# Performance work log

Measured on AMD Instinct MI355X. Metric: run time of the kernel, lower is better.

## Reference

```python
import jax, jax.numpy as jnp
import numpy as np

B, T, S, F, H, V = 4, 160, 80, 640, 1024, 1024

def setup_inputs() -> dict:
    key = jax.random.key(0)
    ks = jax.random.split(key, 4)
    return {
        "source_encodings": jax.random.normal(ks[0], (B, T, F), dtype=jnp.float32),
        "target_encodings": jax.random.normal(ks[1], (B, S, F), dtype=jnp.float32),
        "W1": jax.random.normal(ks[2], (F, H), dtype=jnp.float32) * (1.0 / np.sqrt(F)),
        "b1": jnp.zeros((H,), dtype=jnp.float32),
        "W2": jax.random.normal(ks[3], (H, V), dtype=jnp.float32) * (1.0 / np.sqrt(H)),
        "b2": jnp.zeros((V,), dtype=jnp.float32),
    }

def reference(source_encodings, target_encodings, W1, b1, W2, b2):
    # broadcast add: [B,T,1,F] + [B,1,S,F] -> [B,T,S,F]
    combined = source_encodings[:, :, None, :] + target_encodings[:, None, :, :]
    # FFN: Linear -> ReLU -> Linear (dropout=0 / eval)
    h = jax.nn.relu(jnp.einsum("btsf,fh->btsh", combined, W1) + b1)
    logits = jnp.einsum("btsh,hv->btsv", h, W2) + b2
    # eval mode applies log_softmax over vocab
    return jax.nn.log_softmax(logits, axis=-1)
```

## Files before the change

kernel.cpp:

```cpp
#include <hip/hip_runtime.h>
#include <type_traits>
#include <utility>

#define B_ 4
#define T_ 160
#define S_ 80
#define F_ 640
#define H_ 1024
#define V_ 1024

typedef float f32x4 __attribute__((ext_vector_type(4)));
typedef short s16x8 __attribute__((ext_vector_type(8)));
typedef __bf16 bf16x8_t __attribute__((ext_vector_type(8)));

template <typename T, typename = void>
struct MfmaTakes : std::false_type {};
template <typename T>
struct MfmaTakes<T, std::void_t<decltype(__builtin_amdgcn_mfma_f32_16x16x32_bf16(
    std::declval<T>(), std::declval<T>(), std::declval<f32x4>(), 0, 0, 0))>>
    : std::true_type {};

template <typename S8>
__device__ __forceinline__ f32x4 mfma_bf16_16x16x32(S8 a, S8 b, f32x4 c) {
  if constexpr (MfmaTakes<S8>::value) {
    return __builtin_amdgcn_mfma_f32_16x16x32_bf16(a, b, c, 0, 0, 0);
  } else {
    return __builtin_amdgcn_mfma_f32_16x16x32_bf16(
        __builtin_bit_cast(bf16x8_t, a), __builtin_bit_cast(bf16x8_t, b), c, 0, 0, 0);
  }
}

__device__ __forceinline__ unsigned short f2bf(float x) {
  unsigned int u = __float_as_uint(x);
  u += 0x7FFFu + ((u >> 16) & 1u);
  return (unsigned short)(u >> 16);
}

__global__ __launch_bounds__(256) void prep_weights(const float* __restrict__ W1,
                                                    const float* __restrict__ W2,
                                                    s16x8* __restrict__ W1p,
                                                    s16x8* __restrict__ W2p) {
  const int NW1 = (F_ / 8) * H_;
  const int NW2 = (H_ / 8) * V_;
  int c = blockIdx.x * 256 + threadIdx.x;
  if (c < NW1) {
    int kg = c >> 10, v = c & 1023;
    s16x8 o;
#pragma unroll
    for (int i = 0; i < 8; ++i) o[i] = (short)f2bf(W1[(kg * 8 + i) * H_ + v]);
    W1p[c] = o;
  } else if (c < NW1 + NW2) {
    int c2 = c - NW1;
    int kg = c2 >> 10, v = c2 & 1023;
    s16x8 o;
#pragma unroll
    for (int i = 0; i < 8; ++i) o[i] = (short)f2bf(W2[(kg * 8 + i) * V_ + v]);
    W2p[c2] = o;
  }
}

__global__ __launch_bounds__(512, 2) void pq_gemm(const float* __restrict__ src,
                                                  const float* __restrict__ tgt,
                                                  const s16x8* __restrict__ W1p,
                                                  const float* __restrict__ b1,
                                                  float* __restrict__ P,
                                                  float* __restrict__ Q) {
  __shared__ s16x8 a_lds[64 * 80];
  const int tid = threadIdx.x;
  const int wr = blockIdx.x;
  const int r0 = wr * 64;
  const bool isP = (wr < 10);

  for (int c = tid; c < 64 * 80; c += 512) {
    int m = c / 80, kg8 = c - m * 80;
    int R = r0 + m;
    const float* rowp = isP ? (src + R * F_) : (tgt + (R - 640) * F_);
    const f32x4* p4 = (const f32x4*)(rowp + kg8 * 8);
    f32x4 x0 = p4[0], x1 = p4[1];
    s16x8 o;
#pragma unroll
    for (int i = 0; i < 4; ++i) o[i] = (short)f2bf(x0[i]);
#pragma unroll
    for (int i = 0; i < 4; ++i) o[4 + i] = (short)f2bf(x1[i]);
    a_lds[m * 80 + (kg8 ^ (m & 7))] = o;
  }
  __syncthreads();

  const int l = tid & 63, wv = tid >> 6;
  const int g = l >> 4, cl = l & 15;
  const f32x4 zero = {0.f, 0.f, 0.f, 0.f};
  f32x4 acc[4][8];
#pragma unroll
  for (int rt = 0; rt < 4; ++rt)
#pragma unroll
    for (int ct = 0; ct < 8; ++ct) acc[rt][ct] = zero;

  const s16x8* bbase = W1p + g * 1024 + wv * 128 + cl;
  s16x8 bA[8], bB[8], af[4];
#pragma unroll
  for (int ct = 0; ct < 8; ++ct) bA[ct] = bbase[ct * 16];

  for (int ks = 0; ks < 20; ks += 2) {
#pragma unroll
    for (int ct = 0; ct < 8; ++ct) bB[ct] = bbase[(ks + 1) * 4096 + ct * 16];
#pragma unroll
    for (int rt = 0; rt < 4; ++rt) {
      int m = rt * 16 + cl;
      af[rt] = a_lds[m * 80 + ((ks * 4 + g) ^ (m & 7))];
    }
#pragma unroll
    for (int ct = 0; ct < 8; ++ct)
#pragma unroll
      for (int rt = 0; rt < 4; ++rt)
        acc[rt][ct] = mfma_bf16_16x16x32(af[rt], bA[ct], acc[rt][ct]);
    int ksn = (ks + 2 < 20) ? (ks + 2) : 0;
#pragma unroll
    for (int ct = 0; ct < 8; ++ct) bA[ct] = bbase[ksn * 4096 + ct * 16];
#pragma unroll
    for (int rt = 0; rt < 4; ++rt) {
      int m = rt * 16 + cl;
      af[rt] = a_lds[m * 80 + (((ks + 1) * 4 + g) ^ (m & 7))];
    }
#pragma unroll
    for (int ct = 0; ct < 8; ++ct)
#pragma unroll
      for (int rt = 0; rt < 4; ++rt)
        acc[rt][ct] = mfma_bf16_16x16x32(af[rt], bB[ct], acc[rt][ct]);
  }

  float b1v[8];
#pragma unroll
  for (int ct = 0; ct < 8; ++ct) b1v[ct] = isP ? b1[wv * 128 + ct * 16 + cl] : 0.f;
  float* outbase = isP ? P : Q;
  const int orow0 = isP ? r0 : (r0 - 640);
#pragma unroll
  for (int rt = 0; rt < 4; ++rt) {
#pragma unroll
    for (int j = 0; j < 4; ++j) {
      int row = rt * 16 + g * 4 + j;
      float* op = outbase + (size_t)(orow0 + row) * H_ + wv * 128 + cl;
#pragma unroll
      for (int ct = 0; ct < 8; ++ct) op[ct * 16] = acc[rt][ct][j] + b1v[ct];
    }
  }
}

__global__ __launch_bounds__(512, 2) void joint_main(const float* __restrict__ Pm,
                                                     const float* __restrict__ Qm,
                                                     const s16x8* __restrict__ W2p,
                                                     const float* __restrict__ b2,
                                                     float* __restrict__ out) {
  __shared__ s16x8 h_lds[32 * 129];
  const int tid = threadIdx.x;
  int bx = blockIdx.x;
  int bid = (bx & 7) * 200 + (bx >> 3);
  const int b = bid / 400;
  int rem = bid - b * 400;
  const int t0 = (rem / 10) * 4;
  const int s0 = (rem - (rem / 10) * 10) * 8;

  for (int c = tid; c < 32 * 128; c += 512) {
    int m = c >> 7, kg8 = c & 127;
    int dt = m >> 3, ds = m & 7;
    const f32x4* p4 = (const f32x4*)(Pm + (size_t)(b * T_ + t0 + dt) * H_ + kg8 * 8);
    const f32x4* q4 = (const f32x4*)(Qm + (size_t)(b * S_ + s0 + ds) * H_ + kg8 * 8);
    f32x4 x0 = p4[0] + q4[0];
    f32x4 x1 = p4[1] + q4[1];
    s16x8 o;
#pragma unroll
    for (int i = 0; i < 4; ++i) o[i] = (short)f2bf(fmaxf(x0[i], 0.f));
#pragma unroll
    for (int i = 0; i < 4; ++i) o[4 + i] = (short)f2bf(fmaxf(x1[i], 0.f));
    h_lds[m * 129 + kg8] = o;
  }
  __syncthreads();

  const int l = tid & 63, wv = tid >> 6;
  const int g = l >> 4, cl = l & 15;
  f32x4 acc[2][8];
#pragma unroll
  for (int rt = 0; rt < 2; ++rt)
#pragma unroll
    for (int ct = 0; ct < 8; ++ct) acc[rt][ct] = {0.f, 0.f, 0.f, 0.f};

  const s16x8* bb = W2p + g * 1024 + wv * 128 + cl;
  const s16x8* a0p = h_lds + cl * 129 + g;
  const s16x8* a1p = h_lds + (16 + cl) * 129 + g;

  s16x8 b0[4], b1[4], af0, af1;
#pragma unroll
  for (int i = 0; i < 4; ++i) b0[i] = bb[i * 16];
  af0 = a0p[0];
  af1 = a1p[0];

#pragma unroll
  for (int ks = 0; ks < 32; ++ks) {
#pragma unroll
    for (int i = 0; i < 4; ++i) b1[i] = bb[ks * 4096 + 64 + i * 16];
    __builtin_amdgcn_s_setprio(1);
#pragma unroll
    for (int i = 0; i < 4; ++i) {
      acc[0][i] = mfma_bf16_16x16x32(af0, b0[i], acc[0][i]);
      acc[1][i] = mfma_bf16_16x16x32(af1, b0[i], acc[1][i]);
    }
    __builtin_amdgcn_s_setprio(0);
    const int ksn = (ks + 1 < 32) ? ks + 1 : 0;
#pragma unroll
    for (int i = 0; i < 4; ++i) b0[i] = bb[ksn * 4096 + i * 16];
    s16x8 afn0 = a0p[ksn * 4];
    s16x8 afn1 = a1p[ksn * 4];
    __builtin_amdgcn_s_setprio(1);
#pragma unroll
    for (int i = 0; i < 4; ++i) {
      acc[0][4 + i] = mfma_bf16_16x16x32(af0, b1[i], acc[0][4 + i]);
      acc[1][4 + i] = mfma_bf16_16x16x32(af1, b1[i], acc[1][4 + i]);
    }
    __builtin_amdgcn_s_setprio(0);
    af0 = afn0;
    af1 = afn1;
  }

  __syncthreads();
  float* redm = reinterpret_cast<float*>(h_lds);
  float* reds = redm + 256;
  float* gmbuf = reds + 256;
  float* lsebuf = gmbuf + 32;

#pragma unroll
  for (int ct = 0; ct < 8; ++ct) {
    float bv = b2[wv * 128 + ct * 16 + cl];
#pragma unroll
    for (int rt = 0; rt < 2; ++rt)
#pragma unroll
      for (int j = 0; j < 4; ++j) acc[rt][ct][j] += bv;
  }

#pragma unroll
  for (int rt = 0; rt < 2; ++rt)
#pragma unroll
    for (int j = 0; j < 4; ++j) {
      float mx = acc[rt][0][j];
#pragma unroll
      for (int ct = 1; ct < 8; ++ct) mx = fmaxf(mx, acc[rt][ct][j]);
#pragma unroll
      for (int msk = 1; msk < 16; msk <<= 1) mx = fmaxf(mx, __shfl_xor(mx, msk, 64));
      if (cl == 0) redm[wv * 32 + rt * 16 + g * 4 + j] = mx;
    }
  __syncthreads();

  if (tid < 32) {
    float mx = redm[tid];
#pragma unroll
    for (int w = 1; w < 8; ++w) mx = fmaxf(mx, redm[w * 32 + tid]);
    gmbuf[tid] = mx;
  }
  __syncthreads();

#pragma unroll
  for (int rt = 0; rt < 2; ++rt)
#pragma unroll
    for (int j = 0; j < 4; ++j) {
      int row = rt * 16 + g * 4 + j;
      float gm = gmbuf[row];
      float ps = 0.f;
#pragma unroll
      for (int ct = 0; ct < 8; ++ct) ps += __expf(acc[rt][ct][j] - gm);
#pragma unroll
      for (int msk = 1; msk < 16; msk <<= 1) ps += __shfl_xor(ps, msk, 64);
      if (cl == 0) reds[wv * 32 + row] = ps;
    }
  __syncthreads();

  if (tid < 32) {
    float s = reds[tid];
#pragma unroll
    for (int w = 1; w < 8; ++w) s += reds[w * 32 + tid];
    lsebuf[tid] = gmbuf[tid] + __logf(s);
  }
  __syncthreads();

#pragma unroll
  for (int rt = 0; rt < 2; ++rt)
#pragma unroll
    for (int j = 0; j < 4; ++j) {
      int row = rt * 16 + g * 4 + j;
      float lse = lsebuf[row];
      int n = (b * T_ + t0 + (row >> 3)) * S_ + s0 + (row & 7);
      float* op = out + (size_t)n * V_ + wv * 128 + cl;
#pragma unroll
      for (int ct = 0; ct < 8; ++ct) op[ct * 16] = acc[rt][ct][j] - lse;
    }
}

extern "C" void kernel_launch(void* const* d_in, const int* in_sizes, int n_in,
                              void* d_out, int out_size, void* d_ws, size_t ws_size,
                              hipStream_t stream) {
  const float* src = (const float*)d_in[0];
  const float* tgt = (const float*)d_in[1];
  const float* W1  = (const float*)d_in[2];
  const float* b1  = (const float*)d_in[3];
  const float* W2  = (const float*)d_in[4];
  const float* b2  = (const float*)d_in[5];
  float* out = (float*)d_out;

  char* ws = (char*)d_ws;
  s16x8* W1p = (s16x8*)(ws);
  s16x8* W2p = (s16x8*)(ws + 1310720);
  float* P   = (float*)(ws + 3407872);
  float* Q   = (float*)(ws + 6029312);

  prep_weights<<<832, 256, 0, stream>>>(W1, W2, W1p, W2p);
  pq_gemm<<<15, 512, 0, stream>>>(src, tgt, W1p, b1, P, Q);
  joint_main<<<1600, 512, 0, stream>>>(P, Q, W2p, b2, out);
}
```

Before: 201.2 us.

## Double the joint kernel's row tile to 64 rows per block to reuse W2

Each joint_main block now handles 8 t by 8 s (64 output rows) instead of 4 by 8, so every W2 fragment loaded from global memory feeds four MFMA row tiles instead of two. This halves total W2 traffic, and the grid drops from 1600 to 800 blocks. The B-fragment prefetch is restructured into full 8-wide current/next buffers, and the setprio interleaving is removed. The cost is roughly double the accumulator and fragment registers and LDS, which may drop occupancy below the declared 2 blocks per CU or cause spills, plus fewer blocks to balance across CUs.

```diff
diff --git a/kernel.cpp b/kernel.cpp
--- a/kernel.cpp
+++ b/kernel.cpp
@@ -150,16 +150,16 @@
                                                      const s16x8* __restrict__ W2p,
                                                      const float* __restrict__ b2,
                                                      float* __restrict__ out) {
-  __shared__ s16x8 h_lds[32 * 129];
+  __shared__ s16x8 h_lds[64 * 129];
   const int tid = threadIdx.x;
   int bx = blockIdx.x;
-  int bid = (bx & 7) * 200 + (bx >> 3);
-  const int b = bid / 400;
-  int rem = bid - b * 400;
-  const int t0 = (rem / 10) * 4;
+  int bid = (bx & 7) * 100 + (bx >> 3);
+  const int b = bid / 200;
+  int rem = bid - b * 200;
+  const int t0 = (rem / 10) * 8;
   const int s0 = (rem - (rem / 10) * 10) * 8;
 
-  for (int c = tid; c < 32 * 128; c += 512) {
+  for (int c = tid; c < 64 * 128; c += 512) {
     int m = c >> 7, kg8 = c & 127;
     int dt = m >> 3, ds = m & 7;
     const f32x4* p4 = (const f32x4*)(Pm + (size_t)(b * T_ + t0 + dt) * H_ + kg8 * 8);
@@ -177,66 +177,59 @@
 
   const int l = tid & 63, wv = tid >> 6;
   const int g = l >> 4, cl = l & 15;
-  f32x4 acc[2][8];
-#pragma unroll
-  for (int rt = 0; rt < 2; ++rt)
+  f32x4 acc[4][8];
+#pragma unroll
+  for (int rt = 0; rt < 4; ++rt)
 #pragma unroll
     for (int ct = 0; ct < 8; ++ct) acc[rt][ct] = {0.f, 0.f, 0.f, 0.f};
 
   const s16x8* bb = W2p + g * 1024 + wv * 128 + cl;
-  const s16x8* a0p = h_lds + cl * 129 + g;
-  const s16x8* a1p = h_lds + (16 + cl) * 129 + g;
-
-  s16x8 b0[4], b1[4], af0, af1;
-#pragma unroll
-  for (int i = 0; i < 4; ++i) b0[i] = bb[i * 16];
-  af0 = a0p[0];
-  af1 = a1p[0];
-
-#pragma unroll
+  const s16x8* a0p = h_lds + (0 * 16 + cl) * 129 + g;
+  const s16x8* a1p = h_lds + (1 * 16 + cl) * 129 + g;
+  const s16x8* a2p = h_lds + (2 * 16 + cl) * 129 + g;
+  const s16x8* a3p = h_lds + (3 * 16 + cl) * 129 + g;
+
+  s16x8 bcur[8], bnxt[8], af[4], afn[4];
+#pragma unroll
+  for (int i = 0; i < 8; ++i) bcur[i] = bb[i * 16];
+  af[0] = a0p[0]; af[1] = a1p[0]; af[2] = a2p[0]; af[3] = a3p[0];
+
+#pragma unroll 4
   for (int ks = 0; ks < 32; ++ks) {
-#pragma unroll
-    for (int i = 0; i < 4; ++i) b1[i] = bb[ks * 4096 + 64 + i * 16];
-    __builtin_amdgcn_s_setprio(1);
-#pragma unroll
-    for (int i = 0; i < 4; ++i) {
-      acc[0][i] = mfma_bf16_16x16x32(af0, b0[i], acc[0][i]);
-      acc[1][i] = mfma_bf16_16x16x32(af1, b0[i], acc[1][i]);
-    }
-    __builtin_amdgcn_s_setprio(0);
     const int ksn = (ks + 1 < 32) ? ks + 1 : 0;
-#pragma unroll
-    for (int i = 0; i < 4; ++i) b0[i] = bb[ksn * 4096 + i * 16];
-    s16x8 afn0 = a0p[ksn * 4];
-    s16x8 afn1 = a1p[ksn * 4];
-    __builtin_amdgcn_s_setprio(1);
-#pragma unroll
-    for (int i = 0; i < 4; ++i) {
-      acc[0][4 + i] = mfma_bf16_16x16x32(af0, b1[i], acc[0][4 + i]);
-      acc[1][4 + i] = mfma_bf16_16x16x32(af1, b1[i], acc[1][4 + i]);
-    }
-    __builtin_amdgcn_s_setprio(0);
-    af0 = afn0;
-    af1 = afn1;
+    const s16x8* nb = bb + ksn * 4096;
+#pragma unroll
+    for (int i = 0; i < 8; ++i) bnxt[i] = nb[i * 16];
+    afn[0] = a0p[ksn * 4]; afn[1] = a1p[ksn * 4];
+    afn[2] = a2p[ksn * 4]; afn[3] = a3p[ksn * 4];
+#pragma unroll
+    for (int ct = 0; ct < 8; ++ct)
+#pragma unroll
+      for (int rt = 0; rt < 4; ++rt)
+        acc[rt][ct] = mfma_bf16_16x16x32(af[rt], bcur[ct], acc[rt][ct]);
+#pragma unroll
+    for (int i = 0; i < 8; ++i) bcur[i] = bnxt[i];
+#pragma unroll
+    for (int rt = 0; rt < 4; ++rt) af[rt] = afn[rt];
   }
 
   __syncthreads();
   float* redm = reinterpret_cast<float*>(h_lds);
-  float* reds = redm + 256;
-  float* gmbuf = reds + 256;
-  float* lsebuf = gmbuf + 32;
+  float* reds = redm + 512;
+  float* gmbuf = reds + 512;
+  float* lsebuf = gmbuf + 64;
 
 #pragma unroll
   for (int ct = 0; ct < 8; ++ct) {
     float bv = b2[wv * 128 + ct * 16 + cl];
 #pragma unroll
-    for (int rt = 0; rt < 2; ++rt)
+    for (int rt = 0; rt < 4; ++rt)
 #pragma unroll
       for (int j = 0; j < 4; ++j) acc[rt][ct][j] += bv;
   }
 
 #pragma unroll
-  for (int rt = 0; rt < 2; ++rt)
+  for (int rt = 0; rt < 4; ++rt)
 #pragma unroll
     for (int j = 0; j < 4; ++j) {
       float mx = acc[rt][0][j];
@@ -244,20 +237,20 @@
       for (int ct = 1; ct < 8; ++ct) mx = fmaxf(mx, acc[rt][ct][j]);
 #pragma unroll
       for (int msk = 1; msk < 16; msk <<= 1) mx = fmaxf(mx, __shfl_xor(mx, msk, 64));
-      if (cl == 0) redm[wv * 32 + rt * 16 + g * 4 + j] = mx;
-    }
-  __syncthreads();
-
-  if (tid < 32) {
+      if (cl == 0) redm[wv * 64 + rt * 16 + g * 4 + j] = mx;
+    }
+  __syncthreads();
+
+  if (tid < 64) {
     float mx = redm[tid];
 #pragma unroll
-    for (int w = 1; w < 8; ++w) mx = fmaxf(mx, redm[w * 32 + tid]);
+    for (int w = 1; w < 8; ++w) mx = fmaxf(mx, redm[w * 64 + tid]);
     gmbuf[tid] = mx;
   }
   __syncthreads();
 
 #pragma unroll
-  for (int rt = 0; rt < 2; ++rt)
+  for (int rt = 0; rt < 4; ++rt)
 #pragma unroll
     for (int j = 0; j < 4; ++j) {
       int row = rt * 16 + g * 4 + j;
@@ -267,20 +260,20 @@
       for (int ct = 0; ct < 8; ++ct) ps += __expf(acc[rt][ct][j] - gm);
 #pragma unroll
       for (int msk = 1; msk < 16; msk <<= 1) ps += __shfl_xor(ps, msk, 64);
-      if (cl == 0) reds[wv * 32 + row] = ps;
-    }
-  __syncthreads();
-
-  if (tid < 32) {
+      if (cl == 0) reds[wv * 64 + row] = ps;
+    }
+  __syncthreads();
+
+  if (tid < 64) {
     float s = reds[tid];
 #pragma unroll
-    for (int w = 1; w < 8; ++w) s += reds[w * 32 + tid];
+    for (int w = 1; w < 8; ++w) s += reds[w * 64 + tid];
     lsebuf[tid] = gmbuf[tid] + __logf(s);
   }
   __syncthreads();
 
 #pragma unroll
-  for (int rt = 0; rt < 2; ++rt)
+  for (int rt = 0; rt < 4; ++rt)
 #pragma unroll
     for (int j = 0; j < 4; ++j) {
       int row = rt * 16 + g * 4 + j;
@@ -311,5 +304,5 @@
 
   prep_weights<<<832, 256, 0, stream>>>(W1, W2, W1p, W2p);
   pq_gemm<<<15, 512, 0, stream>>>(src, tgt, W1p, b1, P, Q);
-  joint_main<<<1600, 512, 0, stream>>>(P, Q, W2p, b2, out);
-}
+  joint_main<<<800, 512, 0, stream>>>(P, Q, W2p, b2, out);
+}
```

After: 280.8 us. +39.6%, slower.

## Split joint_main vocab across 16 waves and drop manual software pipelining

Applied to the files above, without the earlier changes.

joint_main now launches 1024 threads per block, so each of 16 waves covers 64 vocab columns instead of 8 waves covering 128. The accumulator footprint halves, the launch bounds move to (1024, 8), and the reduction buffers grow to hold 16 per-wave partials. The hand-written double-buffered B/A prefetch and s_setprio hints are replaced by a plain loop with unroll 2, leaving load scheduling to the compiler. The aim is more resident waves to hide W2 load latency, at the cost of losing explicit prefetch overlap and adding a longer cross-wave reduction.

```diff
diff --git a/kernel.cpp b/kernel.cpp
--- a/kernel.cpp
+++ b/kernel.cpp
@@ -145,11 +145,11 @@
   }
 }
 
-__global__ __launch_bounds__(512, 2) void joint_main(const float* __restrict__ Pm,
-                                                     const float* __restrict__ Qm,
-                                                     const s16x8* __restrict__ W2p,
-                                                     const float* __restrict__ b2,
-                                                     float* __restrict__ out) {
+__global__ __launch_bounds__(1024, 8) void joint_main(const float* __restrict__ Pm,
+                                                      const float* __restrict__ Qm,
+                                                      const s16x8* __restrict__ W2p,
+                                                      const float* __restrict__ b2,
+                                                      float* __restrict__ out) {
   __shared__ s16x8 h_lds[32 * 129];
   const int tid = threadIdx.x;
   int bx = blockIdx.x;
@@ -159,7 +159,7 @@
   const int t0 = (rem / 10) * 4;
   const int s0 = (rem - (rem / 10) * 10) * 8;
 
-  for (int c = tid; c < 32 * 128; c += 512) {
+  for (int c = tid; c < 32 * 128; c += 1024) {
     int m = c >> 7, kg8 = c & 127;
     int dt = m >> 3, ds = m & 7;
     const f32x4* p4 = (const f32x4*)(Pm + (size_t)(b * T_ + t0 + dt) * H_ + kg8 * 8);
@@ -177,58 +177,44 @@
 
   const int l = tid & 63, wv = tid >> 6;
   const int g = l >> 4, cl = l & 15;
-  f32x4 acc[2][8];
-#pragma unroll
-  for (int rt = 0; rt < 2; ++rt)
-#pragma unroll
-    for (int ct = 0; ct < 8; ++ct) acc[rt][ct] = {0.f, 0.f, 0.f, 0.f};
-
-  const s16x8* bb = W2p + g * 1024 + wv * 128 + cl;
+  f32x4 acc[2][4];
+#pragma unroll
+  for (int rt = 0; rt < 2; ++rt)
+#pragma unroll
+    for (int ct = 0; ct < 4; ++ct) acc[rt][ct] = {0.f, 0.f, 0.f, 0.f};
+
+  const s16x8* bb = W2p + g * 1024 + wv * 64 + cl;
   const s16x8* a0p = h_lds + cl * 129 + g;
   const s16x8* a1p = h_lds + (16 + cl) * 129 + g;
 
-  s16x8 b0[4], b1[4], af0, af1;
-#pragma unroll
-  for (int i = 0; i < 4; ++i) b0[i] = bb[i * 16];
-  af0 = a0p[0];
-  af1 = a1p[0];
-
-#pragma unroll
+#pragma unroll 2
   for (int ks = 0; ks < 32; ++ks) {
-#pragma unroll
-    for (int i = 0; i < 4; ++i) b1[i] = bb[ks * 4096 + 64 + i * 16];
-    __builtin_amdgcn_s_setprio(1);
-#pragma unroll
-    for (int i = 0; i < 4; ++i) {
-      acc[0][i] = mfma_bf16_16x16x32(af0, b0[i], acc[0][i]);
-      acc[1][i] = mfma_bf16_16x16x32(af1, b0[i], acc[1][i]);
-    }
-    __builtin_amdgcn_s_setprio(0);
-    const int ksn = (ks + 1 < 32) ? ks + 1 : 0;
-#pragma unroll
-    for (int i = 0; i < 4; ++i) b0[i] = bb[ksn * 4096 + i * 16];
-    s16x8 afn0 = a0p[ksn * 4];
-    s16x8 afn1 = a1p[ksn * 4];
-    __builtin_amdgcn_s_setprio(1);
-#pragma unroll
-    for (int i = 0; i < 4; ++i) {
-      acc[0][4 + i] = mfma_bf16_16x16x32(af0, b1[i], acc[0][4 + i]);
-      acc[1][4 + i] = mfma_bf16_16x16x32(af1, b1[i], acc[1][4 + i]);
-    }
-    __builtin_amdgcn_s_setprio(0);
-    af0 = afn0;
-    af1 = afn1;
+    const s16x8* base = bb + ks * 4096;
+    s16x8 bf0 = base[0];
+    s16x8 bf1 = base[16];
+    s16x8 bf2 = base[32];
+    s16x8 bf3 = base[48];
+    s16x8 a0 = a0p[ks * 4];
+    s16x8 a1 = a1p[ks * 4];
+    acc[0][0] = mfma_bf16_16x16x32(a0, bf0, acc[0][0]);
+    acc[1][0] = mfma_bf16_16x16x32(a1, bf0, acc[1][0]);
+    acc[0][1] = mfma_bf16_16x16x32(a0, bf1, acc[0][1]);
+    acc[1][1] = mfma_bf16_16x16x32(a1, bf1, acc[1][1]);
+    acc[0][2] = mfma_bf16_16x16x32(a0, bf2, acc[0][2]);
+    acc[1][2] = mfma_bf16_16x16x32(a1, bf2, acc[1][2]);
+    acc[0][3] = mfma_bf16_16x16x32(a0, bf3, acc[0][3]);
+    acc[1][3] = mfma_bf16_16x16x32(a1, bf3, acc[1][3]);
   }
 
   __syncthreads();
   float* redm = reinterpret_cast<float*>(h_lds);
-  float* reds = redm + 256;
-  float* gmbuf = reds + 256;
+  float* reds = redm + 512;
+  float* gmbuf = reds + 512;
   float* lsebuf = gmbuf + 32;
 
 #pragma unroll
-  for (int ct = 0; ct < 8; ++ct) {
-    float bv = b2[wv * 128 + ct * 16 + cl];
+  for (int ct = 0; ct < 4; ++ct) {
+    float bv = b2[wv * 64 + ct * 16 + cl];
 #pragma unroll
     for (int rt = 0; rt < 2; ++rt)
 #pragma unroll
@@ -239,9 +225,8 @@
   for (int rt = 0; rt < 2; ++rt)
 #pragma unroll
     for (int j = 0; j < 4; ++j) {
-      float mx = acc[rt][0][j];
-#pragma unroll
-      for (int ct = 1; ct < 8; ++ct) mx = fmaxf(mx, acc[rt][ct][j]);
+      float mx = fmaxf(fmaxf(acc[rt][0][j], acc[rt][1][j]),
+                       fmaxf(acc[rt][2][j], acc[rt][3][j]));
 #pragma unroll
       for (int msk = 1; msk < 16; msk <<= 1) mx = fmaxf(mx, __shfl_xor(mx, msk, 64));
       if (cl == 0) redm[wv * 32 + rt * 16 + g * 4 + j] = mx;
@@ -251,7 +236,7 @@
   if (tid < 32) {
     float mx = redm[tid];
 #pragma unroll
-    for (int w = 1; w < 8; ++w) mx = fmaxf(mx, redm[w * 32 + tid]);
+    for (int w = 1; w < 16; ++w) mx = fmaxf(mx, redm[w * 32 + tid]);
     gmbuf[tid] = mx;
   }
   __syncthreads();
@@ -262,9 +247,8 @@
     for (int j = 0; j < 4; ++j) {
       int row = rt * 16 + g * 4 + j;
       float gm = gmbuf[row];
-      float ps = 0.f;
-#pragma unroll
-      for (int ct = 0; ct < 8; ++ct) ps += __expf(acc[rt][ct][j] - gm);
+      float ps = __expf(acc[rt][0][j] - gm) + __expf(acc[rt][1][j] - gm) +
+                 __expf(acc[rt][2][j] - gm) + __expf(acc[rt][3][j] - gm);
 #pragma unroll
       for (int msk = 1; msk < 16; msk <<= 1) ps += __shfl_xor(ps, msk, 64);
       if (cl == 0) reds[wv * 32 + row] = ps;
@@ -274,7 +258,7 @@
   if (tid < 32) {
     float s = reds[tid];
 #pragma unroll
-    for (int w = 1; w < 8; ++w) s += reds[w * 32 + tid];
+    for (int w = 1; w < 16; ++w) s += reds[w * 32 + tid];
     lsebuf[tid] = gmbuf[tid] + __logf(s);
   }
   __syncthreads();
@@ -286,9 +270,9 @@
       int row = rt * 16 + g * 4 + j;
       float lse = lsebuf[row];
       int n = (b * T_ + t0 + (row >> 3)) * S_ + s0 + (row & 7);
-      float* op = out + (size_t)n * V_ + wv * 128 + cl;
-#pragma unroll
-      for (int ct = 0; ct < 8; ++ct) op[ct * 16] = acc[rt][ct][j] - lse;
+      float* op = out + (size_t)n * V_ + wv * 64 + cl;
+#pragma unroll
+      for (int ct = 0; ct < 4; ++ct) op[ct * 16] = acc[rt][ct][j] - lse;
     }
 }
 
@@ -311,5 +295,5 @@
 
   prep_weights<<<832, 256, 0, stream>>>(W1, W2, W1p, W2p);
   pq_gemm<<<15, 512, 0, stream>>>(src, tgt, W1p, b1, P, Q);
-  joint_main<<<1600, 512, 0, stream>>>(P, Q, W2p, b2, out);
-}
+  joint_main<<<1600, 1024, 0, stream>>>(P, Q, W2p, b2, out);
+}
```

Measured after the change: 254.3 us. 26.4% more time.

## Split P/Q projection GEMM into 120 smaller tiles for more parallelism

Applied to the files above, without the earlier changes.

The P/Q projection GEMM previously ran on only 15 workgroups with 64-row by 1024-column tiles each. It is now split into 32-row by 256-column tiles across 120 workgroups so more compute units take part. The LDS layout changes from an XOR swizzle to a padded row stride of 81. The trade-off is that each workgroup re-converts its A rows once per column tile, and the explicit double-buffered B prefetch is removed.

```diff
diff --git a/kernel.cpp b/kernel.cpp
--- a/kernel.cpp
+++ b/kernel.cpp
@@ -65,84 +65,65 @@
                                                   const float* __restrict__ b1,
                                                   float* __restrict__ P,
                                                   float* __restrict__ Q) {
-  __shared__ s16x8 a_lds[64 * 80];
+  __shared__ s16x8 a_lds[32 * 81];
   const int tid = threadIdx.x;
-  const int wr = blockIdx.x;
-  const int r0 = wr * 64;
-  const bool isP = (wr < 10);
-
-  for (int c = tid; c < 64 * 80; c += 512) {
+  const int wg = blockIdx.x;
+  const int rowtile = wg >> 2, coltile = wg & 3;
+  const int r0 = rowtile * 32;
+  const bool isP = (r0 < 640);
+  const float* rowbase = isP ? (src + (size_t)r0 * F_) : (tgt + (size_t)(r0 - 640) * F_);
+
+  for (int c = tid; c < 32 * 80; c += 512) {
     int m = c / 80, kg8 = c - m * 80;
-    int R = r0 + m;
-    const float* rowp = isP ? (src + R * F_) : (tgt + (R - 640) * F_);
-    const f32x4* p4 = (const f32x4*)(rowp + kg8 * 8);
+    const f32x4* p4 = (const f32x4*)(rowbase + (size_t)m * F_ + kg8 * 8);
     f32x4 x0 = p4[0], x1 = p4[1];
     s16x8 o;
 #pragma unroll
     for (int i = 0; i < 4; ++i) o[i] = (short)f2bf(x0[i]);
 #pragma unroll
     for (int i = 0; i < 4; ++i) o[4 + i] = (short)f2bf(x1[i]);
-    a_lds[m * 80 + (kg8 ^ (m & 7))] = o;
+    a_lds[m * 81 + kg8] = o;
   }
   __syncthreads();
 
   const int l = tid & 63, wv = tid >> 6;
   const int g = l >> 4, cl = l & 15;
-  const f32x4 zero = {0.f, 0.f, 0.f, 0.f};
-  f32x4 acc[4][8];
-#pragma unroll
-  for (int rt = 0; rt < 4; ++rt)
-#pragma unroll
-    for (int ct = 0; ct < 8; ++ct) acc[rt][ct] = zero;
-
-  const s16x8* bbase = W1p + g * 1024 + wv * 128 + cl;
-  s16x8 bA[8], bB[8], af[4];
-#pragma unroll
-  for (int ct = 0; ct < 8; ++ct) bA[ct] = bbase[ct * 16];
-
-  for (int ks = 0; ks < 20; ks += 2) {
-#pragma unroll
-    for (int ct = 0; ct < 8; ++ct) bB[ct] = bbase[(ks + 1) * 4096 + ct * 16];
-#pragma unroll
-    for (int rt = 0; rt < 4; ++rt) {
-      int m = rt * 16 + cl;
-      af[rt] = a_lds[m * 80 + ((ks * 4 + g) ^ (m & 7))];
-    }
-#pragma unroll
-    for (int ct = 0; ct < 8; ++ct)
-#pragma unroll
-      for (int rt = 0; rt < 4; ++rt)
-        acc[rt][ct] = mfma_bf16_16x16x32(af[rt], bA[ct], acc[rt][ct]);
-    int ksn = (ks + 2 < 20) ? (ks + 2) : 0;
-#pragma unroll
-    for (int ct = 0; ct < 8; ++ct) bA[ct] = bbase[ksn * 4096 + ct * 16];
-#pragma unroll
-    for (int rt = 0; rt < 4; ++rt) {
-      int m = rt * 16 + cl;
-      af[rt] = a_lds[m * 80 + (((ks + 1) * 4 + g) ^ (m & 7))];
-    }
-#pragma unroll
-    for (int ct = 0; ct < 8; ++ct)
-#pragma unroll
-      for (int rt = 0; rt < 4; ++rt)
-        acc[rt][ct] = mfma_bf16_16x16x32(af[rt], bB[ct], acc[rt][ct]);
-  }
-
-  float b1v[8];
-#pragma unroll
-  for (int ct = 0; ct < 8; ++ct) b1v[ct] = isP ? b1[wv * 128 + ct * 16 + cl] : 0.f;
-  float* outbase = isP ? P : Q;
-  const int orow0 = isP ? r0 : (r0 - 640);
-#pragma unroll
-  for (int rt = 0; rt < 4; ++rt) {
+  f32x4 acc[2][2];
+#pragma unroll
+  for (int rt = 0; rt < 2; ++rt)
+#pragma unroll
+    for (int ct = 0; ct < 2; ++ct) acc[rt][ct] = {0.f, 0.f, 0.f, 0.f};
+
+  const s16x8* bb = W1p + g * 1024 + coltile * 256 + wv * 32 + cl;
+  const s16x8* a0p = a_lds + cl * 81 + g;
+  const s16x8* a1p = a_lds + (16 + cl) * 81 + g;
+
+#pragma unroll
+  for (int ks = 0; ks < 20; ++ks) {
+    s16x8 b0 = bb[ks * 4096];
+    s16x8 b1f = bb[ks * 4096 + 16];
+    s16x8 a0 = a0p[ks * 4];
+    s16x8 a1 = a1p[ks * 4];
+    acc[0][0] = mfma_bf16_16x16x32(a0, b0, acc[0][0]);
+    acc[1][0] = mfma_bf16_16x16x32(a1, b0, acc[1][0]);
+    acc[0][1] = mfma_bf16_16x16x32(a0, b1f, acc[0][1]);
+    acc[1][1] = mfma_bf16_16x16x32(a1, b1f, acc[1][1]);
+  }
+
+  float bv[2];
+#pragma unroll
+  for (int ct = 0; ct < 2; ++ct)
+    bv[ct] = isP ? b1[coltile * 256 + wv * 32 + ct * 16 + cl] : 0.f;
+  float* outbase = isP ? (P + (size_t)r0 * H_) : (Q + (size_t)(r0 - 640) * H_);
+#pragma unroll
+  for (int rt = 0; rt < 2; ++rt)
 #pragma unroll
     for (int j = 0; j < 4; ++j) {
       int row = rt * 16 + g * 4 + j;
-      float* op = outbase + (size_t)(orow0 + row) * H_ + wv * 128 + cl;
-#pragma unroll
-      for (int ct = 0; ct < 8; ++ct) op[ct * 16] = acc[rt][ct][j] + b1v[ct];
-    }
-  }
+      float* op = outbase + (size_t)row * H_ + coltile * 256 + wv * 32 + cl;
+      op[0] = acc[rt][0][j] + bv[0];
+      op[16] = acc[rt][1][j] + bv[1];
+    }
 }
 
 __global__ __launch_bounds__(512, 2) void joint_main(const float* __restrict__ Pm,
@@ -310,6 +291,6 @@
   float* Q   = (float*)(ws + 6029312);
 
   prep_weights<<<832, 256, 0, stream>>>(W1, W2, W1p, W2p);
-  pq_gemm<<<15, 512, 0, stream>>>(src, tgt, W1p, b1, P, Q);
+  pq_gemm<<<120, 512, 0, stream>>>(src, tgt, W1p, b1, P, Q);
   joint_main<<<1600, 512, 0, stream>>>(P, Q, W2p, b2, out);
 }
```

New measurement: 177.4 us. 11.8% less time.
